# Performance work log

Measured on AMD Instinct MI355X. Metric: run time of the kernel, lower is better.

The kernel has to match this reference:

```python
import jax, jax.numpy as jnp
import numpy as np

BLOCK_SIZE = 256
NEG = -10000.0  # matches the module's additive mask constant (not -inf)

def setup_inputs() -> dict:
    key = jax.random.key(0)
    qkv = jax.random.normal(key, (4, 4096, 192), dtype=jnp.float32)
    return {"qkv": qkv}

def reference(qkv):
    B, S, dm = qkv.shape
    d = dm // 3
    q, k, v = qkv[..., :d], qkv[..., d:2*d], qkv[..., 2*d:]
    scale = 1.0 / jnp.sqrt(jnp.asarray(d, dtype=qkv.dtype))
    scores = jnp.einsum('bqd,bkd->bqk', q, k * scale)  # [B,S,S]
    i = jnp.arange(S)[:, None]
    j = jnp.arange(S)[None, :]
    # allowed: i - block_size <= j <= i ; else additive -10000 (as in torch code)
    mask = jnp.where((j <= i) & (j >= i - BLOCK_SIZE), 0.0, NEG).astype(scores.dtype)
    attn = jax.nn.softmax(scores + mask[None, :, :], axis=-1)
    return jnp.einsum('bqk,bkd->bqd', attn, v)
```

## Files before the change

kernel.cpp:

```cpp
#include <hip/hip_runtime.h>
#include <hip/hip_bf16.h>


#define LOG2E 1.4426950408889634f

typedef __attribute__((ext_vector_type(8))) short  frag;
typedef __attribute__((ext_vector_type(4))) float  f32x4;

static __device__ inline short f2bf(float x) {
    __hip_bfloat16 h = __float2bfloat16(x);
    return __builtin_bit_cast(short, h);
}

#define DPPF(x, ctrl) __builtin_bit_cast(float, \
    __builtin_amdgcn_mov_dpp(__builtin_bit_cast(int, (x)), (ctrl), 0xF, 0xF, true))

static __device__ inline float red16_max(float x) {
    x = fmaxf(x, DPPF(x, 0xB1));
    x = fmaxf(x, DPPF(x, 0x4E));
    x = fmaxf(x, DPPF(x, 0x141));
    x = fmaxf(x, DPPF(x, 0x140));
    return x;
}
static __device__ inline float red16_sum(float x) {
    x += DPPF(x, 0xB1);
    x += DPPF(x, 0x4E);
    x += DPPF(x, 0x141);
    x += DPPF(x, 0x140);
    return x;
}

#define LSTR 72
#define VSTR 328
#define PSTR 40
#define OSTR 65

__global__ __launch_bounds__(512, 2) void swa_mfma3(const float* __restrict__ qkv,
                                                    float* __restrict__ out)
{
    __shared__ short Qs[64 * LSTR];
    __shared__ short Ks[320 * LSTR];
    __shared__ short Vt[64 * VSTR];
    __shared__ short Pw[8][16 * PSTR];
    __shared__ float Om[4][16 * OSTR];
    __shared__ float2 mlbuf[4][16];

    const int b    = blockIdx.y;
    const int q0   = blockIdx.x * 64;
    const int t    = threadIdx.x;
    const int w    = t >> 6;
    const int s    = w & 3;
    const int g    = w >> 2;
    const int lane = t & 63;
    const int cl   = lane & 15;
    const int quad = lane >> 4;
    const int ql   = 4 * quad;

    const float4* qkv4 = (const float4*)qkv;
    const int r_st = t >> 3;
    const int c8   = t & 7;

    const int c0 = (q0 >= 256) ? 0 : (4 - (q0 >> 6));

    {
        const size_t base = (size_t)(b * 4096 + q0 + r_st) * 48;
        #pragma unroll
        for (int i = 0; i < 2; ++i) {
            float4 v = qkv4[base + c8 + 8 * i];
            short4 s4 = { f2bf(v.x * 0.125f), f2bf(v.y * 0.125f),
                          f2bf(v.z * 0.125f), f2bf(v.w * 0.125f) };
            *(short4*)&Qs[r_st * LSTR + 4 * (c8 + 8 * i)] = s4;
        }
    }

    const int kbase = b * 4096 + q0 - 256;
    #pragma unroll
    for (int c = 0; c < 5; ++c) {
        if (c < c0) continue;
        const size_t base = (size_t)(kbase + 64 * c + r_st) * 48;
        #pragma unroll
        for (int i = 0; i < 2; ++i) {
            float4 kv = qkv4[base + 16 + c8 + 8 * i];
            float4 vv = qkv4[base + 32 + c8 + 8 * i];
            short4 k4 = { f2bf(kv.x), f2bf(kv.y), f2bf(kv.z), f2bf(kv.w) };
            *(short4*)&Ks[(64 * c + r_st) * LSTR + 4 * (c8 + 8 * i)] = k4;
            const int d0 = 4 * (c8 + 8 * i);
            Vt[(d0 + 0) * VSTR + 64 * c + r_st] = f2bf(vv.x);
            Vt[(d0 + 1) * VSTR + 64 * c + r_st] = f2bf(vv.y);
            Vt[(d0 + 2) * VSTR + 64 * c + r_st] = f2bf(vv.z);
            Vt[(d0 + 3) * VSTR + 64 * c + r_st] = f2bf(vv.w);
        }
    }

    __syncthreads();

    const frag qf0 = *(const frag*)&Qs[(16 * s + cl) * LSTR + 8 * quad];
    const frag qf1 = *(const frag*)&Qs[(16 * s + cl) * LSTR + 32 + 8 * quad];

    float m[4], l[4];
    f32x4 oacc[4];
    #pragma unroll
    for (int r = 0; r < 4; ++r) { m[r] = -1e30f; l[r] = 0.f; }
    #pragma unroll
    for (int n4 = 0; n4 < 4; ++n4) oacc[n4] = (f32x4){0.f, 0.f, 0.f, 0.f};

    #pragma unroll
    for (int c = 0; c < 5; ++c) {
        if (c < c0) continue;

        f32x4 sc[2];
        #pragma unroll
        for (int u = 0; u < 2; ++u) {
            const int t4 = 2 * g + u;
            const int krow = 64 * c + 16 * t4;
            sc[u] = (f32x4){0.f, 0.f, 0.f, 0.f};
            const frag kf0 = *(const frag*)&Ks[(krow + cl) * LSTR + 8 * quad];
            const frag kf1 = *(const frag*)&Ks[(krow + cl) * LSTR + 32 + 8 * quad];
            sc[u] = __builtin_amdgcn_mfma_f32_16x16x32_bf16(qf0, kf0, sc[u], 0, 0, 0);
            sc[u] = __builtin_amdgcn_mfma_f32_16x16x32_bf16(qf1, kf1, sc[u], 0, 0, 0);
        }

        if (c == 4) {
            #pragma unroll
            for (int u = 0; u < 2; ++u) {
                const int t4 = 2 * g + u;
                #pragma unroll
                for (int r = 0; r < 4; ++r)
                    if (16 * s + ql + r < 16 * t4 + cl) sc[u][r] = -1e30f;
            }
        } else if (c == 0) {
            #pragma unroll
            for (int u = 0; u < 2; ++u) {
                const int t4 = 2 * g + u;
                #pragma unroll
                for (int r = 0; r < 4; ++r)
                    if (16 * s + ql + r > 16 * t4 + cl) sc[u][r] = -1e30f;
            }
        }

        #pragma unroll
        for (int r = 0; r < 4; ++r) {
            float mx = red16_max(fmaxf(sc[0][r], sc[1][r]));
            const float mnew  = fmaxf(m[r], mx);
            const float alpha = __builtin_amdgcn_exp2f((m[r] - mnew) * LOG2E);
            m[r] = mnew;
            float sum = 0.f;
            #pragma unroll
            for (int u = 0; u < 2; ++u) {
                float p = (sc[u][r] <= -1e29f)
                            ? 0.f
                            : __builtin_amdgcn_exp2f((sc[u][r] - mnew) * LOG2E);
                Pw[w][(ql + r) * PSTR + 16 * u + cl] = f2bf(p);
                sum += p;
            }
            l[r] = l[r] * alpha + red16_sum(sum);
            #pragma unroll
            for (int n4 = 0; n4 < 4; ++n4) oacc[n4][r] *= alpha;
        }

        const frag pf = *(const frag*)&Pw[w][cl * PSTR + 8 * quad];
        #pragma unroll
        for (int n4 = 0; n4 < 4; ++n4) {
            const frag vf = *(const frag*)&Vt[(16 * n4 + cl) * VSTR + 64 * c + 32 * g + 8 * quad];
            oacc[n4] = __builtin_amdgcn_mfma_f32_16x16x32_bf16(pf, vf, oacc[n4], 0, 0, 0);
        }
    }

    if (g == 1) {
        #pragma unroll
        for (int n4 = 0; n4 < 4; ++n4)
            #pragma unroll
            for (int r = 0; r < 4; ++r)
                Om[s][(ql + r) * OSTR + 16 * n4 + cl] = oacc[n4][r];
        if (cl == 0)
            #pragma unroll
            for (int r = 0; r < 4; ++r)
                mlbuf[s][ql + r] = make_float2(m[r], l[r]);
    }
    __syncthreads();
    if (g == 0) {
        #pragma unroll
        for (int r = 0; r < 4; ++r) {
            const float2 ml1 = mlbuf[s][ql + r];
            const float M  = fmaxf(m[r], ml1.x);
            const float a0 = __builtin_amdgcn_exp2f((m[r]  - M) * LOG2E);
            const float a1 = __builtin_amdgcn_exp2f((ml1.x - M) * LOG2E);
            const float L  = l[r] * a0 + ml1.y * a1;
            const float inv = 1.0f / L;
            const size_t row = (size_t)(b * 4096 + q0 + 16 * s + ql + r) * 64;
            #pragma unroll
            for (int n4 = 0; n4 < 4; ++n4) {
                const float o1 = Om[s][(ql + r) * OSTR + 16 * n4 + cl];
                out[row + 16 * n4 + cl] = (oacc[n4][r] * a0 + o1 * a1) * inv;
            }
        }
    }
}

extern "C" void kernel_launch(void* const* d_in, const int* in_sizes, int n_in,
                              void* d_out, int out_size, void* d_ws, size_t ws_size,
                              hipStream_t stream) {
    const float* qkv = (const float*)d_in[0];
    float* out = (float*)d_out;
    dim3 grid(64, 4);
    dim3 block(512);
    hipLaunchKernelGGL(swa_mfma3, grid, block, 0, stream, qkv, out);
}
```

Measured before the change: 70.30 us.

## Halve query tile, stream K/V in 128-row chunks with register prefetch

```diff
diff --git a/kernel.cpp b/kernel.cpp
--- a/kernel.cpp
+++ b/kernel.cpp
@@ -30,72 +30,80 @@
     return x;
 }
 
-#define LSTR 72
-#define VSTR 328
+#define KSTR 72
+#define VSTR 136
 #define PSTR 40
 #define OSTR 65
 
-__global__ __launch_bounds__(512, 2) void swa_mfma3(const float* __restrict__ qkv,
+__global__ __launch_bounds__(512, 4) void swa_mfma5(const float* __restrict__ qkv,
                                                     float* __restrict__ out)
 {
-    __shared__ short Qs[64 * LSTR];
-    __shared__ short Ks[320 * LSTR];
+    __shared__ short Qs[32 * KSTR];
+    __shared__ short Ks[128 * KSTR];
     __shared__ short Vt[64 * VSTR];
     __shared__ short Pw[8][16 * PSTR];
-    __shared__ float Om[4][16 * OSTR];
-    __shared__ float2 mlbuf[4][16];
-
-    const int b    = blockIdx.y;
-    const int q0   = blockIdx.x * 64;
+    __shared__ float Om[2][3][16 * OSTR];
+    __shared__ float2 mlbuf[2][3][16];
+
+    const int b   = blockIdx.y;
+    const int xb  = blockIdx.x;
+    const int qb  = 16 * (xb & 7) + (xb >> 3);
+    const int q0  = qb * 32;
+
     const int t    = threadIdx.x;
     const int w    = t >> 6;
-    const int s    = w & 3;
-    const int g    = w >> 2;
+    const int s    = w & 1;
+    const int g    = w >> 1;
     const int lane = t & 63;
     const int cl   = lane & 15;
     const int quad = lane >> 4;
     const int ql   = 4 * quad;
 
     const float4* qkv4 = (const float4*)qkv;
-    const int r_st = t >> 3;
-    const int c8   = t & 7;
-
-    const int c0 = (q0 >= 256) ? 0 : (4 - (q0 >> 6));
+
+    const int r2 = t >> 2;
+    const int c4 = t & 3;
+    const int rq = t >> 4;
+    const int cq = t & 15;
+
+    const int lo0 = 256 - q0;
+    const int lo1 = (128 - q0 > 0) ? (128 - q0) : 0;
+    const int it_first = (q0 > 128) ? 0 : ((q0 > 0) ? 1 : 2);
 
     {
-        const size_t base = (size_t)(b * 4096 + q0 + r_st) * 48;
-        #pragma unroll
-        for (int i = 0; i < 2; ++i) {
-            float4 v = qkv4[base + c8 + 8 * i];
-            short4 s4 = { f2bf(v.x * 0.125f), f2bf(v.y * 0.125f),
-                          f2bf(v.z * 0.125f), f2bf(v.w * 0.125f) };
-            *(short4*)&Qs[r_st * LSTR + 4 * (c8 + 8 * i)] = s4;
-        }
-    }
-
-    const int kbase = b * 4096 + q0 - 256;
-    #pragma unroll
-    for (int c = 0; c < 5; ++c) {
-        if (c < c0) continue;
-        const size_t base = (size_t)(kbase + 64 * c + r_st) * 48;
-        #pragma unroll
-        for (int i = 0; i < 2; ++i) {
-            float4 kv = qkv4[base + 16 + c8 + 8 * i];
-            float4 vv = qkv4[base + 32 + c8 + 8 * i];
-            short4 k4 = { f2bf(kv.x), f2bf(kv.y), f2bf(kv.z), f2bf(kv.w) };
-            *(short4*)&Ks[(64 * c + r_st) * LSTR + 4 * (c8 + 8 * i)] = k4;
-            const int d0 = 4 * (c8 + 8 * i);
-            Vt[(d0 + 0) * VSTR + 64 * c + r_st] = f2bf(vv.x);
-            Vt[(d0 + 1) * VSTR + 64 * c + r_st] = f2bf(vv.y);
-            Vt[(d0 + 2) * VSTR + 64 * c + r_st] = f2bf(vv.z);
-            Vt[(d0 + 3) * VSTR + 64 * c + r_st] = f2bf(vv.w);
-        }
-    }
-
-    __syncthreads();
-
-    const frag qf0 = *(const frag*)&Qs[(16 * s + cl) * LSTR + 8 * quad];
-    const frag qf1 = *(const frag*)&Qs[(16 * s + cl) * LSTR + 32 + 8 * quad];
+        const size_t base = (size_t)(b * 4096 + q0 + rq) * 48;
+        float4 v = qkv4[base + cq];
+        short4 s4 = { f2bf(v.x * 0.125f), f2bf(v.y * 0.125f),
+                      f2bf(v.z * 0.125f), f2bf(v.w * 0.125f) };
+        *(short4*)&Qs[rq * KSTR + 4 * cq] = s4;
+    }
+
+    float4 pK[4], pV[4];
+    auto prefetch = [&](int itx) {
+        bool valid;
+        size_t base;
+        if (itx == 2) {
+            valid = (r2 < 32);
+            base = (size_t)(b * 4096 + q0 + (r2 & 31)) * 48;
+        } else {
+            valid = true;
+            int rg = q0 - 256 + 128 * itx + r2;
+            rg = rg < 0 ? 0 : rg;
+            base = (size_t)(b * 4096 + rg) * 48;
+        }
+        #pragma unroll
+        for (int i = 0; i < 4; ++i) {
+            if (valid) {
+                pK[i] = qkv4[base + 16 + c4 + 4 * i];
+                pV[i] = qkv4[base + 32 + c4 + 4 * i];
+            } else {
+                pK[i] = make_float4(0.f, 0.f, 0.f, 0.f);
+                pV[i] = make_float4(0.f, 0.f, 0.f, 0.f);
+            }
+        }
+    };
+
+    prefetch(it_first);
 
     float m[4], l[4];
     f32x4 oacc[4];
@@ -105,36 +113,69 @@
     for (int n4 = 0; n4 < 4; ++n4) oacc[n4] = (f32x4){0.f, 0.f, 0.f, 0.f};
 
     #pragma unroll
-    for (int c = 0; c < 5; ++c) {
-        if (c < c0) continue;
+    for (int it = 0; it < 3; ++it) {
+        if (it < it_first) continue;
+
+        __syncthreads();
+
+        #pragma unroll
+        for (int i = 0; i < 4; ++i) {
+            short4 k4 = { f2bf(pK[i].x), f2bf(pK[i].y),
+                          f2bf(pK[i].z), f2bf(pK[i].w) };
+            *(short4*)&Ks[r2 * KSTR + 4 * (c4 + 4 * i)] = k4;
+            const int d0 = 4 * (c4 + 4 * i);
+            Vt[(d0 + 0) * VSTR + r2] = f2bf(pV[i].x);
+            Vt[(d0 + 1) * VSTR + r2] = f2bf(pV[i].y);
+            Vt[(d0 + 2) * VSTR + r2] = f2bf(pV[i].z);
+            Vt[(d0 + 3) * VSTR + r2] = f2bf(pV[i].w);
+        }
+        __syncthreads();
+
+        if (it < 2) prefetch(it + 1);
+
+        const frag qf0 = *(const frag*)&Qs[(16 * s + cl) * KSTR + 8 * quad];
+        const frag qf1 = *(const frag*)&Qs[(16 * s + cl) * KSTR + 32 + 8 * quad];
 
         f32x4 sc[2];
         #pragma unroll
         for (int u = 0; u < 2; ++u) {
-            const int t4 = 2 * g + u;
-            const int krow = 64 * c + 16 * t4;
+            const int krow = 32 * g + 16 * u;
             sc[u] = (f32x4){0.f, 0.f, 0.f, 0.f};
-            const frag kf0 = *(const frag*)&Ks[(krow + cl) * LSTR + 8 * quad];
-            const frag kf1 = *(const frag*)&Ks[(krow + cl) * LSTR + 32 + 8 * quad];
+            const frag kf0 = *(const frag*)&Ks[(krow + cl) * KSTR + 8 * quad];
+            const frag kf1 = *(const frag*)&Ks[(krow + cl) * KSTR + 32 + 8 * quad];
             sc[u] = __builtin_amdgcn_mfma_f32_16x16x32_bf16(qf0, kf0, sc[u], 0, 0, 0);
             sc[u] = __builtin_amdgcn_mfma_f32_16x16x32_bf16(qf1, kf1, sc[u], 0, 0, 0);
         }
 
-        if (c == 4) {
+        if (it == 0) {
             #pragma unroll
             for (int u = 0; u < 2; ++u) {
-                const int t4 = 2 * g + u;
-                #pragma unroll
-                for (int r = 0; r < 4; ++r)
-                    if (16 * s + ql + r < 16 * t4 + cl) sc[u][r] = -1e30f;
-            }
-        } else if (c == 0) {
+                const int o = 32 * g + 16 * u + cl;
+                #pragma unroll
+                for (int r = 0; r < 4; ++r) {
+                    const int rb = 16 * s + ql + r;
+                    if (o < rb || o < lo0) sc[u][r] = -1e30f;
+                }
+            }
+        } else if (it == 1) {
+            if (lo1 > 0) {
+                #pragma unroll
+                for (int u = 0; u < 2; ++u) {
+                    const int o = 32 * g + 16 * u + cl;
+                    #pragma unroll
+                    for (int r = 0; r < 4; ++r)
+                        if (o < lo1) sc[u][r] = -1e30f;
+                }
+            }
+        } else {
             #pragma unroll
             for (int u = 0; u < 2; ++u) {
-                const int t4 = 2 * g + u;
-                #pragma unroll
-                for (int r = 0; r < 4; ++r)
-                    if (16 * s + ql + r > 16 * t4 + cl) sc[u][r] = -1e30f;
+                const int o = 32 * g + 16 * u + cl;
+                #pragma unroll
+                for (int r = 0; r < 4; ++r) {
+                    const int rb = 16 * s + ql + r;
+                    if (o > rb) sc[u][r] = -1e30f;
+                }
             }
         }
 
@@ -161,38 +202,49 @@
         const frag pf = *(const frag*)&Pw[w][cl * PSTR + 8 * quad];
         #pragma unroll
         for (int n4 = 0; n4 < 4; ++n4) {
-            const frag vf = *(const frag*)&Vt[(16 * n4 + cl) * VSTR + 64 * c + 32 * g + 8 * quad];
+            const frag vf = *(const frag*)&Vt[(16 * n4 + cl) * VSTR + 32 * g + 8 * quad];
             oacc[n4] = __builtin_amdgcn_mfma_f32_16x16x32_bf16(pf, vf, oacc[n4], 0, 0, 0);
         }
     }
 
-    if (g == 1) {
+    if (g != 0) {
         #pragma unroll
         for (int n4 = 0; n4 < 4; ++n4)
             #pragma unroll
             for (int r = 0; r < 4; ++r)
-                Om[s][(ql + r) * OSTR + 16 * n4 + cl] = oacc[n4][r];
+                Om[s][g - 1][(ql + r) * OSTR + 16 * n4 + cl] = oacc[n4][r];
         if (cl == 0)
             #pragma unroll
             for (int r = 0; r < 4; ++r)
-                mlbuf[s][ql + r] = make_float2(m[r], l[r]);
+                mlbuf[s][g - 1][ql + r] = make_float2(m[r], l[r]);
     }
     __syncthreads();
     if (g == 0) {
         #pragma unroll
         for (int r = 0; r < 4; ++r) {
-            const float2 ml1 = mlbuf[s][ql + r];
-            const float M  = fmaxf(m[r], ml1.x);
-            const float a0 = __builtin_amdgcn_exp2f((m[r]  - M) * LOG2E);
-            const float a1 = __builtin_amdgcn_exp2f((ml1.x - M) * LOG2E);
-            const float L  = l[r] * a0 + ml1.y * a1;
+            float M = m[r];
+            float L = l[r];
+            float acc[4];
+            #pragma unroll
+            for (int n4 = 0; n4 < 4; ++n4) acc[n4] = oacc[n4][r];
+            #pragma unroll
+            for (int p = 0; p < 3; ++p) {
+                const float2 ml = mlbuf[s][p][ql + r];
+                const float Mn = fmaxf(M, ml.x);
+                const float a0 = __builtin_amdgcn_exp2f((M    - Mn) * LOG2E);
+                const float a1 = __builtin_amdgcn_exp2f((ml.x - Mn) * LOG2E);
+                L = L * a0 + ml.y * a1;
+                #pragma unroll
+                for (int n4 = 0; n4 < 4; ++n4)
+                    acc[n4] = acc[n4] * a0
+                            + Om[s][p][(ql + r) * OSTR + 16 * n4 + cl] * a1;
+                M = Mn;
+            }
             const float inv = 1.0f / L;
             const size_t row = (size_t)(b * 4096 + q0 + 16 * s + ql + r) * 64;
             #pragma unroll
-            for (int n4 = 0; n4 < 4; ++n4) {
-                const float o1 = Om[s][(ql + r) * OSTR + 16 * n4 + cl];
-                out[row + 16 * n4 + cl] = (oacc[n4][r] * a0 + o1 * a1) * inv;
-            }
+            for (int n4 = 0; n4 < 4; ++n4)
+                out[row + 16 * n4 + cl] = acc[n4] * inv;
         }
     }
 }
@@ -202,7 +254,7 @@
                               hipStream_t stream) {
     const float* qkv = (const float*)d_in[0];
     float* out = (float*)d_out;
-    dim3 grid(64, 4);
+    dim3 grid(128, 4);
     dim3 block(512);
-    hipLaunchKernelGGL(swa_mfma3, grid, block, 0, stream, qkv, out);
-}
+    hipLaunchKernelGGL(swa_mfma5, grid, block, 0, stream, qkv, out);
+}
```

After: 74.19 us. +5.5%, slower.
